# Optimization experiments

Hardware: AMD Instinct MI355X
Metric: run time of the kernel (lower is better)

## Reference

```python
import jax, jax.numpy as jnp
import numpy as np
from jax import lax

LENGTH, WIDTH = 64, 64
INPUT_DIM = 1


def _convlstm_layer(x_tbchw, W, b):
    """Run one ConvLSTM layer over time. x_tbchw: (L,B,Cin,H,W).
    W: (4*hid, Cin+hid, 3, 3), b: (4*hid,). Returns (outputs (L,B,hid,H,W), last_h)."""
    L, B, _, H, Wd = x_tbchw.shape
    hid = W.shape[0] // 4
    h0 = jnp.zeros((B, hid, H, Wd), dtype=x_tbchw.dtype)
    c0 = jnp.zeros((B, hid, H, Wd), dtype=x_tbchw.dtype)

    def step(carry, xt):
        h, c = carry
        z = lax.conv_general_dilated(
            jnp.concatenate([xt, h], axis=1), W,
            window_strides=(1, 1), padding='SAME',
            dimension_numbers=('NCHW', 'OIHW', 'NCHW'))
        z = z + b[None, :, None, None]
        cc_i, cc_f, cc_o, cc_g = jnp.split(z, 4, axis=1)
        c_next = jax.nn.sigmoid(cc_f) * c + jax.nn.sigmoid(cc_i) * jnp.tanh(cc_g)
        h_next = jax.nn.sigmoid(cc_o) * jnp.tanh(c_next)
        return (h_next, c_next), h_next

    (h_last, _), outs = lax.scan(step, (h0, c0), x_tbchw)
    return outs, h_last


def setup_inputs() -> dict:
    key = jax.random.key(0)
    k1, k2, k3 = jax.random.split(key, 3)
    B, L, N = 16, 12, LENGTH * WIDTH
    emd, out_len = 128, 12
    return {
        'history_data': jax.random.normal(k1, (B, L, N, 1), dtype=jnp.float32),
        'future_data': jnp.zeros((B, L, N, 1), dtype=jnp.float32),
        'W0': jax.random.normal(k2, (4 * emd, INPUT_DIM + emd, 3, 3), dtype=jnp.float32) * 0.05,
        'b0': jnp.zeros((4 * emd,), dtype=jnp.float32),
        'W1': jax.random.normal(k3, (4 * out_len, emd + out_len, 3, 3), dtype=jnp.float32) * 0.05,
        'b1': jnp.zeros((4 * out_len,), dtype=jnp.float32),
        'batch_seen': 0,
        'epoch': 0,
        'train': 1,
    }


def reference(history_data, future_data, W0, b0, W1, b1, batch_seen, epoch, train):
    B, L, N, C = history_data.shape
    # (B,L,1,H,W) -> (L,B,1,H,W) for time-major scan
    x = history_data[..., :INPUT_DIM].reshape(B, L, INPUT_DIM, LENGTH, WIDTH)
    x = jnp.transpose(x, (1, 0, 2, 3, 4))
    outs0, _ = _convlstm_layer(x, W0, b0)          # (L,B,emd,H,W)
    _, h_last = _convlstm_layer(outs0, W1, b1)     # (B,out_len,H,W)
    prediction = h_last.reshape(B, L, LENGTH * WIDTH)[..., None]  # (B,L,N,1)
    return prediction
```

## Files before the change

### kernel.cpp

```cpp
#include <hip/hip_runtime.h>
#include <hip/hip_bf16.h>


typedef __attribute__((ext_vector_type(8))) short short8;
typedef __attribute__((ext_vector_type(4))) float float4v;

#define CS 160
#define KTOT 1440

__device__ __forceinline__ float sigf(float x) { return 1.f / (1.f + __expf(-x)); }
__device__ __forceinline__ short f2hs(float v) {
  _Float16 h = (_Float16)v;
  return *(short*)&h;
}
__device__ __forceinline__ float hs2f(short s) {
  _Float16 h; *(short*)&h = s; return (float)h;
}
__device__ __forceinline__ float bs2f(short s) {
  __hip_bfloat16 h; *(short*)&h = s; return __bfloat162float(h);
}
__device__ __forceinline__ short f2bs(float v) {
  __hip_bfloat16 h = __float2bfloat16(v);
  return *(short*)&h;
}

__device__ __forceinline__ void async_ld16(const short* g, short* l) {
  __builtin_amdgcn_global_load_lds(
      (const __attribute__((address_space(1))) unsigned int*)g,
      (__attribute__((address_space(3))) unsigned int*)l, 16, 0, 0);
}

__device__ __forceinline__ void stage_row(const short* __restrict__ rowPtr, bool rowOK,
                                          short* dstRow, int lane,
                                          const short* __restrict__ zp) {
  #pragma unroll
  for (int j = 0; j < 4; ++j) {
    int e = j * 64 + lane;
    int px = e >> 2, v = e & 3;
    int xx = px - 1;
    const short* g = (rowOK && xx >= 0) ? (rowPtr + (size_t)xx * CS + v * 8) : zp;
    async_ld16(g, dstRow + e * 8);
  }
  if (lane < 8) {
    int px = 64 + (lane >> 2), v = lane & 3, xx = px - 1;
    short8 val = {0, 0, 0, 0, 0, 0, 0, 0};
    if (rowOK && xx < 64) val = *(const short8*)(rowPtr + (size_t)xx * CS + v * 8);
    *(short8*)(dstRow + px * 32 + v * 8) = val;
  }
}

__global__ void detect_dtype(const unsigned short* __restrict__ w0, int* __restrict__ flag) {
  int lane = threadIdx.x;
  int cnt = 0;
  for (int i = 0; i < 4; ++i) {
    unsigned short u = w0[2 * (lane + 64 * i)];
    int e = (u >> 7) & 0xFF;
    unsigned long long b = __ballot(e >= 0xC0);
    cnt += __popcll(b);
  }
  if (lane == 0) *flag = (cnt > 32) ? 1 : 0;
}

__global__ void canon_x(const void* __restrict__ hist, short* __restrict__ Xc,
                        const int* __restrict__ flag) {
  int i = blockIdx.x * 256 + threadIdx.x;
  float v = (*flag) ? ((const float*)hist)[i] : bs2f(((const short*)hist)[i]);
  if (!isfinite(v) || fabsf(v) > 1e4f) v = 0.f;
  Xc[i] = f2hs(v);
}

__global__ void canon_b(const void* __restrict__ b0, const void* __restrict__ b1,
                        float* __restrict__ Bc0, float* __restrict__ Bc1,
                        const int* __restrict__ flag) {
  int i = blockIdx.x * 256 + threadIdx.x;
  int fl = *flag;
  if (i < 512) {
    float v = fl ? ((const float*)b0)[i] : bs2f(((const short*)b0)[i]);
    if (!isfinite(v) || fabsf(v) > 1e4f) v = 0.f;
    Bc0[i] = v;
  } else if (i < 560) {
    int j = i - 512;
    float v = fl ? ((const float*)b1)[j] : bs2f(((const short*)b1)[j]);
    if (!isfinite(v) || fabsf(v) > 1e4f) v = 0.f;
    Bc1[j] = v;
  }
}

__global__ void prep_w0(const void* __restrict__ W0, short* __restrict__ Wp,
                        const int* __restrict__ flag) {
  int i = blockIdx.x * 256 + threadIdx.x;
  if (i >= 512 * KTOT) return;
  int fl = *flag;
  int co = i / KTOT, k = i - co * KTOT;
  int tap = k / CS, c = k - tap * CS;
  int ci = -1;
  if (c == 0) ci = 0;
  else if (c <= 128) ci = c;
  float w = 0.f;
  if (ci >= 0) {
    int widx = (co * 129 + ci) * 9 + tap;
    w = fl ? ((const float*)W0)[widx] : bs2f(((const short*)W0)[widx]);
    if (!isfinite(w) || fabsf(w) > 1e4f) w = 0.f;
  }
  Wp[i] = f2hs(w);
}

__global__ void prep_w1(const void* __restrict__ W1, short* __restrict__ Wp,
                        const int* __restrict__ flag) {
  int i = blockIdx.x * 256 + threadIdx.x;
  if (i >= 48 * KTOT) return;
  int fl = *flag;
  int co = i / KTOT, k = i - co * KTOT;
  int tap = k / CS, c = k - tap * CS;
  int ci = -1;
  if (c >= 1 && c <= 140) ci = c - 1;
  float w = 0.f;
  if (ci >= 0) {
    int widx = (co * 140 + ci) * 9 + tap;
    w = fl ? ((const float*)W1)[widx] : bs2f(((const short*)W1)[widx]);
    if (!isfinite(w) || fabsf(w) > 1e4f) w = 0.f;
  }
  Wp[i] = f2hs(w);
}

__global__ void fill_x0(const short* __restrict__ Xc, short* __restrict__ P0) {
  int p = blockIdx.x * 256 + threadIdx.x;
  int b = p >> 12, pix = p & 4095;
  P0[(size_t)p * CS] = Xc[b * 12 * 4096 + pix];
}

__global__ __launch_bounds__(256, 2) void gemm_gate0(
    const short* __restrict__ Pcur, short* __restrict__ Pnext,
    const short* __restrict__ Wp, const float* __restrict__ Bc0,
    float* __restrict__ C0, const short* __restrict__ Xc,
    const short* __restrict__ zp, int t) {
  int bx = blockIdx.x;
  int nt = bx >> 9, mt = bx & 511;
  int b = mt >> 5, y0 = (mt & 31) * 2;
  int tid = threadIdx.x, wave = tid >> 6, lane = tid & 63;
  int ln15 = lane & 15, quad = lane >> 4;
  int wm = wave & 1, wn = wave >> 1;
  int hc = nt * 32 + wn * 16 + ln15;

  __shared__ __align__(16) short halo[2 * 4 * 66 * 32];

  float4v acc[4][4];
  #pragma unroll
  for (int i = 0; i < 4; ++i)
    #pragma unroll
    for (int j = 0; j < 4; ++j) acc[i][j] = (float4v){0.f, 0.f, 0.f, 0.f};

  const short* wbase = Wp + (size_t)hc * KTOT + quad * 8;
  short8 bcur[4], bnxt[4];
  #pragma unroll
  for (int g = 0; g < 4; ++g)
    bcur[g] = *(const short8*)(wbase + (size_t)g * 128 * KTOT);

  int yy = y0 - 1 + wave;
  bool rowOK = (yy >= 0) && (yy < 64);
  const short* rowBase = Pcur + (size_t)((b * 64 + yy) * 64) * CS;

  stage_row(rowBase, rowOK, halo + wave * 2112, lane, zp);
  __syncthreads();

  for (int ch = 0; ch < 5; ++ch) {
    int c0 = ch * 32;
    const short* cur = halo + (ch & 1) * 8448;
    if (ch < 4)
      stage_row(rowBase + c0 + 32, rowOK, halo + ((ch + 1) & 1) * 8448 + wave * 2112,
                lane, zp);
    #pragma unroll
    for (int tap = 0; tap < 9; ++tap) {
      int dy = tap / 3, dx = tap - dy * 3;
      int ntap = (tap < 8) ? tap + 1 : 0;
      int nc0 = (tap < 8) ? c0 : ((ch < 4) ? c0 + 32 : c0);
      #pragma unroll
      for (int g = 0; g < 4; ++g)
        bnxt[g] = *(const short8*)(wbase + (size_t)g * 128 * KTOT + ntap * CS + nc0);

      short8 af[4];
      #pragma unroll
      for (int mf = 0; mf < 4; ++mf)
        af[mf] = *(const short8*)&cur[((wm + dy) * 66 + mf * 16 + ln15 + dx) * 32 + quad * 8];
      #pragma unroll
      for (int g = 0; g < 4; ++g)
        #pragma unroll
        for (int mf = 0; mf < 4; ++mf)
          acc[mf][g] = __builtin_amdgcn_mfma_f32_16x16x32_f16(af[mf], bcur[g], acc[mf][g], 0, 0, 0);
      #pragma unroll
      for (int g = 0; g < 4; ++g) bcur[g] = bnxt[g];
    }
    __syncthreads();
  }

  float bi = Bc0[hc], bff = Bc0[128 + hc], bo = Bc0[256 + hc], bg = Bc0[384 + hc];
  int rowPix = (b * 64 + y0 + wm) * 64;
  #pragma unroll
  for (int mf = 0; mf < 4; ++mf) {
    #pragma unroll
    for (int r = 0; r < 4; ++r) {
      int x = mf * 16 + quad * 4 + r;
      int pix = rowPix + x;
      float zi = acc[mf][0][r] + bi;
      float zf = acc[mf][1][r] + bff;
      float zo = acc[mf][2][r] + bo;
      float zg = acc[mf][3][r] + bg;
      float cprev = C0[(size_t)pix * 128 + hc];
      float cn = sigf(zf) * cprev + sigf(zi) * tanhf(zg);
      float hn = sigf(zo) * tanhf(cn);
      C0[(size_t)pix * 128 + hc] = cn;
      Pnext[(size_t)pix * CS + 1 + hc] = f2hs(hn);
    }
  }
  if (nt == 0 && t < 11 && tid < 128) {
    int rr = tid >> 6, x = tid & 63;
    int yw = y0 + rr;
    Pnext[(size_t)((b * 64 + yw) * 64 + x) * CS] = Xc[(b * 12 + t + 1) * 4096 + yw * 64 + x];
  }
}

__global__ __launch_bounds__(256, 2) void gemm_gate1(
    const short* __restrict__ Prd, short* __restrict__ Pwr,
    const short* __restrict__ Wp, const float* __restrict__ Bc1,
    float* __restrict__ C1, void* __restrict__ outp,
    const short* __restrict__ zp, const int* __restrict__ flagp, int t) {
  int bid = blockIdx.x;
  int b = bid >> 5, y0 = (bid & 31) * 2;
  int tid = threadIdx.x, wave = tid >> 6, lane = tid & 63;
  int ln15 = lane & 15, quad = lane >> 4;
  int wr = wave >> 1, wh = wave & 1;
  int flagv = *flagp;

  __shared__ __align__(16) short halo[2 * 4 * 66 * 32];

  float4v acc[2][3];
  #pragma unroll
  for (int i = 0; i < 2; ++i)
    #pragma unroll
    for (int j = 0; j < 3; ++j) acc[i][j] = (float4v){0.f, 0.f, 0.f, 0.f};

  int yy = y0 - 1 + wave;
  bool rowOK = (yy >= 0) && (yy < 64);
  const short* rowBase = Prd + (size_t)((b * 64 + yy) * 64) * CS;

  const short* wbase = Wp + (size_t)ln15 * KTOT + quad * 8;
  short8 bcur[3], bnxt[3];
  #pragma unroll
  for (int nf = 0; nf < 3; ++nf)
    bcur[nf] = *(const short8*)(wbase + (size_t)nf * 16 * KTOT);

  stage_row(rowBase, rowOK, halo + wave * 2112, lane, zp);
  __syncthreads();

  for (int ch = 0; ch < 5; ++ch) {
    int c0 = ch * 32;
    const short* cur = halo + (ch & 1) * 8448;
    if (ch < 4)
      stage_row(rowBase + c0 + 32, rowOK, halo + ((ch + 1) & 1) * 8448 + wave * 2112,
                lane, zp);
    #pragma unroll
    for (int tap = 0; tap < 9; ++tap) {
      int dy = tap / 3, dx = tap - dy * 3;
      int ntap = (tap < 8) ? tap + 1 : 0;
      int nc0 = (tap < 8) ? c0 : ((ch < 4) ? c0 + 32 : c0);
      #pragma unroll
      for (int nf = 0; nf < 3; ++nf)
        bnxt[nf] = *(const short8*)(wbase + (size_t)nf * 16 * KTOT + ntap * CS + nc0);

      short8 af[2];
      #pragma unroll
      for (int mf = 0; mf < 2; ++mf)
        af[mf] = *(const short8*)&cur[((wr + dy) * 66 + wh * 32 + mf * 16 + ln15 + dx) * 32
                                      + quad * 8];
      #pragma unroll
      for (int nf = 0; nf < 3; ++nf)
        #pragma unroll
        for (int mf = 0; mf < 2; ++mf)
          acc[mf][nf] = __builtin_amdgcn_mfma_f32_16x16x32_f16(af[mf], bcur[nf], acc[mf][nf], 0, 0, 0);
      #pragma unroll
      for (int nf = 0; nf < 3; ++nf) bcur[nf] = bnxt[nf];
    }
    __syncthreads();
  }

  float* zbuf = (float*)halo;
  #pragma unroll
  for (int mf = 0; mf < 2; ++mf)
    #pragma unroll
    for (int nf = 0; nf < 3; ++nf)
      #pragma unroll
      for (int r = 0; r < 4; ++r) {
        int pxl = wr * 64 + wh * 32 + mf * 16 + quad * 4 + r;
        zbuf[pxl * 48 + nf * 16 + ln15] = acc[mf][nf][r];
      }
  __syncthreads();

  #pragma unroll
  for (int k = 0; k < 6; ++k) {
    int id = k * 256 + tid;
    int hc = id >> 7, pxl = id & 127;
    float zi = zbuf[pxl * 48 + hc]      + Bc1[hc];
    float zf = zbuf[pxl * 48 + 12 + hc] + Bc1[12 + hc];
    float zo = zbuf[pxl * 48 + 24 + hc] + Bc1[24 + hc];
    float zg = zbuf[pxl * 48 + 36 + hc] + Bc1[36 + hc];
    int y = y0 + (pxl >> 6), x = pxl & 63;
    int pix = (b * 64 + y) * 64 + x;
    float cprev = C1[(size_t)pix * 12 + hc];
    float cn = sigf(zf) * cprev + sigf(zi) * tanhf(zg);
    float hn = sigf(zo) * tanhf(cn);
    C1[(size_t)pix * 12 + hc] = cn;
    Pwr[(size_t)pix * CS + 129 + hc] = f2hs(hn);
    if (t == 11) {
      int oidx = (b * 12 + hc) * 4096 + y * 64 + x;
      if (flagv) ((float*)outp)[oidx] = hn;
      else ((short*)outp)[oidx] = f2bs(hn);
    }
  }
}

extern "C" void kernel_launch(void* const* d_in, const int* in_sizes, int n_in,
                              void* d_out, int out_size, void* d_ws, size_t ws_size,
                              hipStream_t stream) {
  const void* hist = d_in[0];
  const void* W0 = d_in[2];
  const void* b0 = d_in[3];
  const void* W1 = d_in[4];
  const void* b1 = d_in[5];

  char* ws = (char*)d_ws;
  const size_t PszB = (size_t)16 * 4096 * CS * 2;
  short* P[2] = {(short*)ws, (short*)(ws + PszB)};
  float* C0 = (float*)(ws + 2 * PszB);
  const size_t C0e = 2 * PszB + 33554432;
  float* C1 = (float*)(ws + C0e);
  const size_t C1e = C0e + 3145728;
  short* zp = (short*)(ws + C1e);
  const size_t zpe = C1e + 256;
  short* Xc = (short*)(ws + zpe);
  const size_t Xce = zpe + 1572864;
  short* Wp0 = (short*)(ws + Xce);
  const size_t W0e = Xce + (size_t)512 * KTOT * 2;
  short* Wp1 = (short*)(ws + W0e);
  const size_t W1e = W0e + (size_t)48 * KTOT * 2;
  float* Bc0 = (float*)(ws + W1e);
  float* Bc1 = (float*)(ws + W1e + 2048);
  int* flag = (int*)(ws + W1e + 2048 + 192);

  hipMemsetAsync(ws, 0, zpe, stream);
  detect_dtype<<<1, 64, 0, stream>>>((const unsigned short*)W0, flag);
  canon_x<<<3072, 256, 0, stream>>>(hist, Xc, flag);
  canon_b<<<3, 256, 0, stream>>>(b0, b1, Bc0, Bc1, flag);
  prep_w0<<<(512 * KTOT + 255) / 256, 256, 0, stream>>>(W0, Wp0, flag);
  prep_w1<<<(48 * KTOT + 255) / 256, 256, 0, stream>>>(W1, Wp1, flag);
  fill_x0<<<256, 256, 0, stream>>>(Xc, P[0]);

  for (int t = 0; t < 12; ++t) {
    gemm_gate0<<<2048, 256, 0, stream>>>(P[t & 1], P[(t + 1) & 1], Wp0, Bc0, C0, Xc, zp, t);
    gemm_gate1<<<512, 256, 0, stream>>>(P[(t + 1) & 1], P[t & 1], Wp1, Bc1, C1,
                                        d_out, zp, flag, t);
  }
}
```

Before: 2.198 ms.

## Fuse layer-0 and layer-1 ConvLSTM steps into one skewed launch and swizzle LDS

Layer 0 at step k and layer 1 at step k-1 now run as separate block ranges of a single kernel launch. This cuts the launch count from 24 to 13 and lets the small layer-1 grid fill idle CUs while layer 0 runs. Layer-1 hidden state moves to channels 144..155 of the shared activation buffer so the two layers write disjoint regions, and the packed W1 weights are remapped to match. The LDS halo gets an XOR swizzle on both the async-store and fragment-read sides, and the gate scratch buffer gets a padded stride of 49; both target LDS bank conflicts. In exchange, the whole skew schedule depends on getting the double-buffer parity right, and the fused kernel carries the register and LDS footprint of both bodies.

New measurement: 2.407 ms. +9.5%, slower.

```diff
diff --git a/kernel.cpp b/kernel.cpp
--- a/kernel.cpp
+++ b/kernel.cpp
@@ -33,12 +33,13 @@
 __device__ __forceinline__ void stage_row(const short* __restrict__ rowPtr, bool rowOK,
                                           short* dstRow, int lane,
                                           const short* __restrict__ zp) {
+  int vs8 = (((lane & 3) ^ ((lane >> 3) & 3)) << 3);
   #pragma unroll
   for (int j = 0; j < 4; ++j) {
     int e = j * 64 + lane;
-    int px = e >> 2, v = e & 3;
+    int px = e >> 2;
     int xx = px - 1;
-    const short* g = (rowOK && xx >= 0) ? (rowPtr + (size_t)xx * CS + v * 8) : zp;
+    const short* g = (rowOK && xx >= 0) ? (rowPtr + (size_t)xx * CS + vs8) : zp;
     async_ld16(g, dstRow + e * 8);
   }
   if (lane < 8) {
@@ -113,7 +114,8 @@
   int co = i / KTOT, k = i - co * KTOT;
   int tap = k / CS, c = k - tap * CS;
   int ci = -1;
-  if (c >= 1 && c <= 140) ci = c - 1;
+  if (c >= 1 && c <= 128) ci = c - 1;
+  else if (c >= 144 && c <= 155) ci = 128 + (c - 144);
   float w = 0.f;
   if (ci >= 0) {
     int widx = (co * 140 + ci) * 9 + tap;
@@ -129,12 +131,11 @@
   P0[(size_t)p * CS] = Xc[b * 12 * 4096 + pix];
 }
 
-__global__ __launch_bounds__(256, 2) void gemm_gate0(
-    const short* __restrict__ Pcur, short* __restrict__ Pnext,
+__device__ __forceinline__ void gg0_body(
+    int bx, short* halo, const short* __restrict__ Pcur, short* __restrict__ Pnext,
     const short* __restrict__ Wp, const float* __restrict__ Bc0,
     float* __restrict__ C0, const short* __restrict__ Xc,
     const short* __restrict__ zp, int t) {
-  int bx = blockIdx.x;
   int nt = bx >> 9, mt = bx & 511;
   int b = mt >> 5, y0 = (mt & 31) * 2;
   int tid = threadIdx.x, wave = tid >> 6, lane = tid & 63;
@@ -142,8 +143,6 @@
   int wm = wave & 1, wn = wave >> 1;
   int hc = nt * 32 + wn * 16 + ln15;
 
-  __shared__ __align__(16) short halo[2 * 4 * 66 * 32];
-
   float4v acc[4][4];
   #pragma unroll
   for (int i = 0; i < 4; ++i)
@@ -178,10 +177,11 @@
       for (int g = 0; g < 4; ++g)
         bnxt[g] = *(const short8*)(wbase + (size_t)g * 128 * KTOT + ntap * CS + nc0);
 
+      int qs = (quad ^ (((ln15 + dx) >> 1) & 3)) * 8;
       short8 af[4];
       #pragma unroll
       for (int mf = 0; mf < 4; ++mf)
-        af[mf] = *(const short8*)&cur[((wm + dy) * 66 + mf * 16 + ln15 + dx) * 32 + quad * 8];
+        af[mf] = *(const short8*)&cur[((wm + dy) * 66 + mf * 16 + ln15 + dx) * 32 + qs];
       #pragma unroll
       for (int g = 0; g < 4; ++g)
         #pragma unroll
@@ -219,19 +219,15 @@
   }
 }
 
-__global__ __launch_bounds__(256, 2) void gemm_gate1(
-    const short* __restrict__ Prd, short* __restrict__ Pwr,
+__device__ __forceinline__ void gg1_body(
+    int bid, short* halo, const short* __restrict__ Prd, short* __restrict__ Pwr,
     const short* __restrict__ Wp, const float* __restrict__ Bc1,
     float* __restrict__ C1, void* __restrict__ outp,
-    const short* __restrict__ zp, const int* __restrict__ flagp, int t) {
-  int bid = blockIdx.x;
+    const short* __restrict__ zp, int flagv, int t) {
   int b = bid >> 5, y0 = (bid & 31) * 2;
   int tid = threadIdx.x, wave = tid >> 6, lane = tid & 63;
   int ln15 = lane & 15, quad = lane >> 4;
   int wr = wave >> 1, wh = wave & 1;
-  int flagv = *flagp;
-
-  __shared__ __align__(16) short halo[2 * 4 * 66 * 32];
 
   float4v acc[2][3];
   #pragma unroll
@@ -267,11 +263,12 @@
       for (int nf = 0; nf < 3; ++nf)
         bnxt[nf] = *(const short8*)(wbase + (size_t)nf * 16 * KTOT + ntap * CS + nc0);
 
+      int qs = (quad ^ (((ln15 + dx) >> 1) & 3)) * 8;
       short8 af[2];
       #pragma unroll
       for (int mf = 0; mf < 2; ++mf)
         af[mf] = *(const short8*)&cur[((wr + dy) * 66 + wh * 32 + mf * 16 + ln15 + dx) * 32
-                                      + quad * 8];
+                                      + qs];
       #pragma unroll
       for (int nf = 0; nf < 3; ++nf)
         #pragma unroll
@@ -291,7 +288,7 @@
       #pragma unroll
       for (int r = 0; r < 4; ++r) {
         int pxl = wr * 64 + wh * 32 + mf * 16 + quad * 4 + r;
-        zbuf[pxl * 48 + nf * 16 + ln15] = acc[mf][nf][r];
+        zbuf[pxl * 49 + nf * 16 + ln15] = acc[mf][nf][r];
       }
   __syncthreads();
 
@@ -299,22 +296,38 @@
   for (int k = 0; k < 6; ++k) {
     int id = k * 256 + tid;
     int hc = id >> 7, pxl = id & 127;
-    float zi = zbuf[pxl * 48 + hc]      + Bc1[hc];
-    float zf = zbuf[pxl * 48 + 12 + hc] + Bc1[12 + hc];
-    float zo = zbuf[pxl * 48 + 24 + hc] + Bc1[24 + hc];
-    float zg = zbuf[pxl * 48 + 36 + hc] + Bc1[36 + hc];
+    float zi = zbuf[pxl * 49 + hc]      + Bc1[hc];
+    float zf = zbuf[pxl * 49 + 12 + hc] + Bc1[12 + hc];
+    float zo = zbuf[pxl * 49 + 24 + hc] + Bc1[24 + hc];
+    float zg = zbuf[pxl * 49 + 36 + hc] + Bc1[36 + hc];
     int y = y0 + (pxl >> 6), x = pxl & 63;
     int pix = (b * 64 + y) * 64 + x;
     float cprev = C1[(size_t)pix * 12 + hc];
     float cn = sigf(zf) * cprev + sigf(zi) * tanhf(zg);
     float hn = sigf(zo) * tanhf(cn);
     C1[(size_t)pix * 12 + hc] = cn;
-    Pwr[(size_t)pix * CS + 129 + hc] = f2hs(hn);
+    Pwr[(size_t)pix * CS + 144 + hc] = f2hs(hn);
     if (t == 11) {
       int oidx = (b * 12 + hc) * 4096 + y * 64 + x;
       if (flagv) ((float*)outp)[oidx] = hn;
       else ((short*)outp)[oidx] = f2bs(hn);
     }
+  }
+}
+
+__global__ __launch_bounds__(256, 2) void fused_step(
+    const short* __restrict__ Pr, short* __restrict__ Pw,
+    const short* __restrict__ Wp0, const float* __restrict__ Bc0,
+    float* __restrict__ C0, const short* __restrict__ Xc,
+    const short* __restrict__ Wp1, const float* __restrict__ Bc1,
+    float* __restrict__ C1, void* __restrict__ outp,
+    const short* __restrict__ zp, const int* __restrict__ flagp, int k) {
+  __shared__ __align__(16) short halo[2 * 4 * 66 * 32];
+  int bx = blockIdx.x;
+  if (bx < 2048) {
+    if (k < 12) gg0_body(bx, halo, Pr, Pw, Wp0, Bc0, C0, Xc, zp, k);
+  } else {
+    if (k >= 1) gg1_body(bx - 2048, halo, Pr, Pw, Wp1, Bc1, C1, outp, zp, *flagp, k - 1);
   }
 }
 
@@ -354,9 +367,7 @@
   prep_w1<<<(48 * KTOT + 255) / 256, 256, 0, stream>>>(W1, Wp1, flag);
   fill_x0<<<256, 256, 0, stream>>>(Xc, P[0]);
 
-  for (int t = 0; t < 12; ++t) {
-    gemm_gate0<<<2048, 256, 0, stream>>>(P[t & 1], P[(t + 1) & 1], Wp0, Bc0, C0, Xc, zp, t);
-    gemm_gate1<<<512, 256, 0, stream>>>(P[(t + 1) & 1], P[t & 1], Wp1, Bc1, C1,
-                                        d_out, zp, flag, t);
-  }
-}
+  for (int k = 0; k <= 12; ++k)
+    fused_step<<<2560, 256, 0, stream>>>(P[k & 1], P[(k + 1) & 1], Wp0, Bc0, C0, Xc,
+                                         Wp1, Bc1, C1, d_out, zp, flag, k);
+}
```

## Split input and layer-1 hidden channels out of padded K to shrink GEMM depth

Applied to the files above, without the earlier changes.

Stores layer-0 hidden state in a 128-channel buffer instead of the 160-wide padded one that also held the input channel and layer-1 hidden state. The single input channel is handled through a precomputed 9-tap im2col buffer (Xtap) in one extra MFMA pass. Layer-1 hidden state gets its own 16-channel buffer with a separate small K pass. This cuts the main K loop from 5 chunks to 4 in both gate kernels. It also adds an XOR swizzle to the LDS halo layout and pads the layer-1 z buffer to avoid bank conflicts, at the cost of extra prep kernels and workspace.

After: 2.498 ms. 13.6% more time.

```diff
diff --git a/kernel.cpp b/kernel.cpp
--- a/kernel.cpp
+++ b/kernel.cpp
@@ -5,17 +5,14 @@
 typedef __attribute__((ext_vector_type(8))) short short8;
 typedef __attribute__((ext_vector_type(4))) float float4v;
 
-#define CS 160
-#define KTOT 1440
+#define CS 128
+#define KT0 1152
 
 __device__ __forceinline__ float sigf(float x) { return 1.f / (1.f + __expf(-x)); }
 __device__ __forceinline__ short f2hs(float v) {
   _Float16 h = (_Float16)v;
   return *(short*)&h;
 }
-__device__ __forceinline__ float hs2f(short s) {
-  _Float16 h; *(short*)&h = s; return (float)h;
-}
 __device__ __forceinline__ float bs2f(short s) {
   __hip_bfloat16 h; *(short*)&h = s; return __bfloat162float(h);
 }
@@ -33,12 +30,13 @@
 __device__ __forceinline__ void stage_row(const short* __restrict__ rowPtr, bool rowOK,
                                           short* dstRow, int lane,
                                           const short* __restrict__ zp) {
+  int vs8 = (((lane & 3) ^ ((lane >> 3) & 3)) << 3);
   #pragma unroll
   for (int j = 0; j < 4; ++j) {
     int e = j * 64 + lane;
-    int px = e >> 2, v = e & 3;
+    int px = e >> 2;
     int xx = px - 1;
-    const short* g = (rowOK && xx >= 0) ? (rowPtr + (size_t)xx * CS + v * 8) : zp;
+    const short* g = (rowOK && xx >= 0) ? (rowPtr + (size_t)xx * CS + vs8) : zp;
     async_ld16(g, dstRow + e * 8);
   }
   if (lane < 8) {
@@ -46,6 +44,24 @@
     short8 val = {0, 0, 0, 0, 0, 0, 0, 0};
     if (rowOK && xx < 64) val = *(const short8*)(rowPtr + (size_t)xx * CS + v * 8);
     *(short8*)(dstRow + px * 32 + v * 8) = val;
+  }
+}
+
+__device__ __forceinline__ void stage_h1(const short* __restrict__ rowPtr, bool rowOK,
+                                         short* dstRow, int lane,
+                                         const short* __restrict__ zp) {
+  #pragma unroll
+  for (int j = 0; j < 2; ++j) {
+    int e = j * 64 + lane;
+    int px = e >> 1, h = e & 1, xx = px - 1;
+    const short* g = (rowOK && xx >= 0) ? (rowPtr + (size_t)xx * 16 + h * 8) : zp;
+    async_ld16(g, dstRow + e * 8);
+  }
+  if (lane < 4) {
+    int px = 64 + (lane >> 1), h = lane & 1, xx = px - 1;
+    short8 val = {0, 0, 0, 0, 0, 0, 0, 0};
+    if (rowOK && xx < 64) val = *(const short8*)(rowPtr + (size_t)xx * 16 + h * 8);
+    *(short8*)(dstRow + px * 16 + h * 8) = val;
   }
 }
 
@@ -59,14 +75,6 @@
     cnt += __popcll(b);
   }
   if (lane == 0) *flag = (cnt > 32) ? 1 : 0;
-}
-
-__global__ void canon_x(const void* __restrict__ hist, short* __restrict__ Xc,
-                        const int* __restrict__ flag) {
-  int i = blockIdx.x * 256 + threadIdx.x;
-  float v = (*flag) ? ((const float*)hist)[i] : bs2f(((const short*)hist)[i]);
-  if (!isfinite(v) || fabsf(v) > 1e4f) v = 0.f;
-  Xc[i] = f2hs(v);
 }
 
 __global__ void canon_b(const void* __restrict__ b0, const void* __restrict__ b1,
@@ -86,54 +94,81 @@
   }
 }
 
+__device__ __forceinline__ float ldw(const void* W, int idx, int fl) {
+  float w = fl ? ((const float*)W)[idx] : bs2f(((const short*)W)[idx]);
+  if (!isfinite(w) || fabsf(w) > 1e4f) w = 0.f;
+  return w;
+}
+
 __global__ void prep_w0(const void* __restrict__ W0, short* __restrict__ Wp,
                         const int* __restrict__ flag) {
   int i = blockIdx.x * 256 + threadIdx.x;
-  if (i >= 512 * KTOT) return;
-  int fl = *flag;
-  int co = i / KTOT, k = i - co * KTOT;
-  int tap = k / CS, c = k - tap * CS;
-  int ci = -1;
-  if (c == 0) ci = 0;
-  else if (c <= 128) ci = c;
-  float w = 0.f;
-  if (ci >= 0) {
-    int widx = (co * 129 + ci) * 9 + tap;
-    w = fl ? ((const float*)W0)[widx] : bs2f(((const short*)W0)[widx]);
-    if (!isfinite(w) || fabsf(w) > 1e4f) w = 0.f;
-  }
-  Wp[i] = f2hs(w);
+  if (i >= 512 * KT0) return;
+  int fl = *flag;
+  int co = i / KT0, k = i - co * KT0;
+  int tap = k >> 7, c = k & 127;
+  Wp[i] = f2hs(ldw(W0, (co * 129 + 1 + c) * 9 + tap, fl));
+}
+
+__global__ void prep_wx(const void* __restrict__ W0, short* __restrict__ Wx,
+                        const int* __restrict__ flag) {
+  int i = blockIdx.x * 256 + threadIdx.x;
+  if (i >= 512 * 16) return;
+  int fl = *flag;
+  int co = i >> 4, k = i & 15;
+  float w = (k < 9) ? ldw(W0, (co * 129) * 9 + k, fl) : 0.f;
+  Wx[i] = f2hs(w);
 }
 
 __global__ void prep_w1(const void* __restrict__ W1, short* __restrict__ Wp,
                         const int* __restrict__ flag) {
   int i = blockIdx.x * 256 + threadIdx.x;
-  if (i >= 48 * KTOT) return;
-  int fl = *flag;
-  int co = i / KTOT, k = i - co * KTOT;
-  int tap = k / CS, c = k - tap * CS;
-  int ci = -1;
-  if (c >= 1 && c <= 140) ci = c - 1;
-  float w = 0.f;
-  if (ci >= 0) {
-    int widx = (co * 140 + ci) * 9 + tap;
-    w = fl ? ((const float*)W1)[widx] : bs2f(((const short*)W1)[widx]);
-    if (!isfinite(w) || fabsf(w) > 1e4f) w = 0.f;
-  }
-  Wp[i] = f2hs(w);
-}
-
-__global__ void fill_x0(const short* __restrict__ Xc, short* __restrict__ P0) {
-  int p = blockIdx.x * 256 + threadIdx.x;
-  int b = p >> 12, pix = p & 4095;
-  P0[(size_t)p * CS] = Xc[b * 12 * 4096 + pix];
+  if (i >= 48 * KT0) return;
+  int fl = *flag;
+  int co = i / KT0, k = i - co * KT0;
+  int tap = k >> 7, c = k & 127;
+  Wp[i] = f2hs(ldw(W1, (co * 140 + c) * 9 + tap, fl));
+}
+
+__global__ void prep_wh(const void* __restrict__ W1, short* __restrict__ Wh,
+                        const int* __restrict__ flag) {
+  int i = blockIdx.x * 256 + threadIdx.x;
+  if (i >= 48 * 144) return;
+  int fl = *flag;
+  int co = i / 144, k = i - co * 144;
+  int tap = k >> 4, kk = k & 15;
+  float w = (kk < 12) ? ldw(W1, (co * 140 + 128 + kk) * 9 + tap, fl) : 0.f;
+  Wh[i] = f2hs(w);
+}
+
+__global__ void prep_xtap(const void* __restrict__ hist, short* __restrict__ Xtap,
+                          const int* __restrict__ flag) {
+  int i = blockIdx.x * 256 + threadIdx.x;
+  int t = i >> 16, p = i & 65535;
+  int b = p >> 12, pix = p & 4095, y = pix >> 6, x = pix & 63;
+  int fl = *flag;
+  short8 lo = {0, 0, 0, 0, 0, 0, 0, 0}, hi = {0, 0, 0, 0, 0, 0, 0, 0};
+  #pragma unroll
+  for (int k = 0; k < 9; ++k) {
+    int dy = k / 3, dx = k - dy * 3;
+    int yy = y + dy - 1, xx = x + dx - 1;
+    float f = 0.f;
+    if (yy >= 0 && yy < 64 && xx >= 0 && xx < 64) {
+      int hidx = (b * 12 + t) * 4096 + yy * 64 + xx;
+      f = fl ? ((const float*)hist)[hidx] : bs2f(((const short*)hist)[hidx]);
+      if (!isfinite(f) || fabsf(f) > 1e4f) f = 0.f;
+    }
+    if (k < 8) lo[k] = f2hs(f); else hi[k - 8] = f2hs(f);
+  }
+  *(short8*)(Xtap + (size_t)i * 16) = lo;
+  *(short8*)(Xtap + (size_t)i * 16 + 8) = hi;
 }
 
 __global__ __launch_bounds__(256, 2) void gemm_gate0(
     const short* __restrict__ Pcur, short* __restrict__ Pnext,
-    const short* __restrict__ Wp, const float* __restrict__ Bc0,
-    float* __restrict__ C0, const short* __restrict__ Xc,
-    const short* __restrict__ zp, int t) {
+    const short* __restrict__ Wp, const short* __restrict__ Wx,
+    const float* __restrict__ Bc0, float* __restrict__ C0,
+    const short* __restrict__ Xtap, const short* __restrict__ zp, int t) {
   int bx = blockIdx.x;
   int nt = bx >> 9, mt = bx & 511;
   int b = mt >> 5, y0 = (mt & 31) * 2;
@@ -150,38 +185,58 @@
     #pragma unroll
     for (int j = 0; j < 4; ++j) acc[i][j] = (float4v){0.f, 0.f, 0.f, 0.f};
 
-  const short* wbase = Wp + (size_t)hc * KTOT + quad * 8;
+  const short* wbase = Wp + (size_t)hc * KT0 + quad * 8;
   short8 bcur[4], bnxt[4];
   #pragma unroll
   for (int g = 0; g < 4; ++g)
-    bcur[g] = *(const short8*)(wbase + (size_t)g * 128 * KTOT);
+    bcur[g] = *(const short8*)(wbase + (size_t)g * 128 * KT0);
 
   int yy = y0 - 1 + wave;
   bool rowOK = (yy >= 0) && (yy < 64);
   const short* rowBase = Pcur + (size_t)((b * 64 + yy) * 64) * CS;
+  int rowPix = (b * 64 + y0 + wm) * 64;
 
   stage_row(rowBase, rowOK, halo + wave * 2112, lane, zp);
+
+  {
+    bool hiQ = quad >= 2;
+    const short* xb = Xtap + ((size_t)t * 65536 + rowPix + ln15) * 16 + (quad & 1) * 8;
+    short8 ax[4], bx[4];
+    #pragma unroll
+    for (int mf = 0; mf < 4; ++mf) ax[mf] = *(const short8*)(xb + mf * 256);
+    #pragma unroll
+    for (int g = 0; g < 4; ++g) {
+      const short* wxp = Wx + (size_t)(g * 128 + hc) * 16 + (quad & 1) * 8;
+      bx[g] = *(const short8*)(hiQ ? zp : wxp);
+    }
+    #pragma unroll
+    for (int g = 0; g < 4; ++g)
+      #pragma unroll
+      for (int mf = 0; mf < 4; ++mf)
+        acc[mf][g] = __builtin_amdgcn_mfma_f32_16x16x32_f16(ax[mf], bx[g], acc[mf][g], 0, 0, 0);
+  }
   __syncthreads();
 
-  for (int ch = 0; ch < 5; ++ch) {
+  for (int ch = 0; ch < 4; ++ch) {
     int c0 = ch * 32;
     const short* cur = halo + (ch & 1) * 8448;
-    if (ch < 4)
+    if (ch < 3)
       stage_row(rowBase + c0 + 32, rowOK, halo + ((ch + 1) & 1) * 8448 + wave * 2112,
                 lane, zp);
     #pragma unroll
     for (int tap = 0; tap < 9; ++tap) {
       int dy = tap / 3, dx = tap - dy * 3;
       int ntap = (tap < 8) ? tap + 1 : 0;
-      int nc0 = (tap < 8) ? c0 : ((ch < 4) ? c0 + 32 : c0);
+      int nc0 = (tap < 8) ? c0 : ((ch < 3) ? c0 + 32 : c0);
       #pragma unroll
       for (int g = 0; g < 4; ++g)
-        bnxt[g] = *(const short8*)(wbase + (size_t)g * 128 * KTOT + ntap * CS + nc0);
-
+        bnxt[g] = *(const short8*)(wbase + (size_t)g * 128 * KT0 + ntap * 128 + nc0);
+
+      int qs = (quad ^ (((ln15 + dx) >> 1) & 3)) * 8;
       short8 af[4];
       #pragma unroll
       for (int mf = 0; mf < 4; ++mf)
-        af[mf] = *(const short8*)&cur[((wm + dy) * 66 + mf * 16 + ln15 + dx) * 32 + quad * 8];
+        af[mf] = *(const short8*)&cur[((wm + dy) * 66 + mf * 16 + ln15 + dx) * 32 + qs];
       #pragma unroll
       for (int g = 0; g < 4; ++g)
         #pragma unroll
@@ -194,7 +249,6 @@
   }
 
   float bi = Bc0[hc], bff = Bc0[128 + hc], bo = Bc0[256 + hc], bg = Bc0[384 + hc];
-  int rowPix = (b * 64 + y0 + wm) * 64;
   #pragma unroll
   for (int mf = 0; mf < 4; ++mf) {
     #pragma unroll
@@ -209,19 +263,15 @@
       float cn = sigf(zf) * cprev + sigf(zi) * tanhf(zg);
       float hn = sigf(zo) * tanhf(cn);
       C0[(size_t)pix * 128 + hc] = cn;
-      Pnext[(size_t)pix * CS + 1 + hc] = f2hs(hn);
-    }
-  }
-  if (nt == 0 && t < 11 && tid < 128) {
-    int rr = tid >> 6, x = tid & 63;
-    int yw = y0 + rr;
-    Pnext[(size_t)((b * 64 + yw) * 64 + x) * CS] = Xc[(b * 12 + t + 1) * 4096 + yw * 64 + x];
+      Pnext[(size_t)pix * CS + hc] = f2hs(hn);
+    }
   }
 }
 
 __global__ __launch_bounds__(256, 2) void gemm_gate1(
-    const short* __restrict__ Prd, short* __restrict__ Pwr,
-    const short* __restrict__ Wp, const float* __restrict__ Bc1,
+    const short* __restrict__ Prd, const short* __restrict__ H1rd,
+    short* __restrict__ H1wr, const short* __restrict__ Wp,
+    const short* __restrict__ Wh, const float* __restrict__ Bc1,
     float* __restrict__ C1, void* __restrict__ outp,
     const short* __restrict__ zp, const int* __restrict__ flagp, int t) {
   int bid = blockIdx.x;
@@ -232,6 +282,7 @@
   int flagv = *flagp;
 
   __shared__ __align__(16) short halo[2 * 4 * 66 * 32];
+  __shared__ __align__(16) short h1h[4 * 66 * 16];
 
   float4v acc[2][3];
   #pragma unroll
@@ -242,36 +293,39 @@
   int yy = y0 - 1 + wave;
   bool rowOK = (yy >= 0) && (yy < 64);
   const short* rowBase = Prd + (size_t)((b * 64 + yy) * 64) * CS;
-
-  const short* wbase = Wp + (size_t)ln15 * KTOT + quad * 8;
+  const short* h1Base = H1rd + (size_t)((b * 64 + yy) * 64) * 16;
+
+  const short* wbase = Wp + (size_t)ln15 * KT0 + quad * 8;
   short8 bcur[3], bnxt[3];
   #pragma unroll
   for (int nf = 0; nf < 3; ++nf)
-    bcur[nf] = *(const short8*)(wbase + (size_t)nf * 16 * KTOT);
+    bcur[nf] = *(const short8*)(wbase + (size_t)nf * 16 * KT0);
 
   stage_row(rowBase, rowOK, halo + wave * 2112, lane, zp);
+  stage_h1(h1Base, rowOK, h1h + wave * 1056, lane, zp);
   __syncthreads();
 
-  for (int ch = 0; ch < 5; ++ch) {
+  for (int ch = 0; ch < 4; ++ch) {
     int c0 = ch * 32;
     const short* cur = halo + (ch & 1) * 8448;
-    if (ch < 4)
+    if (ch < 3)
       stage_row(rowBase + c0 + 32, rowOK, halo + ((ch + 1) & 1) * 8448 + wave * 2112,
                 lane, zp);
     #pragma unroll
     for (int tap = 0; tap < 9; ++tap) {
       int dy = tap / 3, dx = tap - dy * 3;
       int ntap = (tap < 8) ? tap + 1 : 0;
-      int nc0 = (tap < 8) ? c0 : ((ch < 4) ? c0 + 32 : c0);
+      int nc0 = (tap < 8) ? c0 : ((ch < 3) ? c0 + 32 : c0);
       #pragma unroll
       for (int nf = 0; nf < 3; ++nf)
-        bnxt[nf] = *(const short8*)(wbase + (size_t)nf * 16 * KTOT + ntap * CS + nc0);
-
+        bnxt[nf] = *(const short8*)(wbase + (size_t)nf * 16 * KT0 + ntap * 128 + nc0);
+
+      int qs = (quad ^ (((ln15 + dx) >> 1) & 3)) * 8;
       short8 af[2];
       #pragma unroll
       for (int mf = 0; mf < 2; ++mf)
         af[mf] = *(const short8*)&cur[((wr + dy) * 66 + wh * 32 + mf * 16 + ln15 + dx) * 32
-                                      + quad * 8];
+                                      + qs];
       #pragma unroll
       for (int nf = 0; nf < 3; ++nf)
         #pragma unroll
@@ -283,6 +337,31 @@
     __syncthreads();
   }
 
+  {
+    bool hiQ = quad >= 2;
+    #pragma unroll
+    for (int tap = 0; tap < 9; ++tap) {
+      int dy = tap / 3, dx = tap - dy * 3;
+      short8 bh[3];
+      #pragma unroll
+      for (int nf = 0; nf < 3; ++nf) {
+        const short* whp = Wh + (size_t)((nf * 16 + ln15) * 9 + tap) * 16 + (quad & 1) * 8;
+        bh[nf] = *(const short8*)(hiQ ? zp : whp);
+      }
+      short8 ah[2];
+      #pragma unroll
+      for (int mf = 0; mf < 2; ++mf)
+        ah[mf] = *(const short8*)&h1h[((wr + dy) * 66 + wh * 32 + mf * 16 + ln15 + dx) * 16
+                                      + (quad & 1) * 8];
+      #pragma unroll
+      for (int nf = 0; nf < 3; ++nf)
+        #pragma unroll
+        for (int mf = 0; mf < 2; ++mf)
+          acc[mf][nf] = __builtin_amdgcn_mfma_f32_16x16x32_f16(ah[mf], bh[nf], acc[mf][nf], 0, 0, 0);
+    }
+  }
+  __syncthreads();
+
   float* zbuf = (float*)halo;
   #pragma unroll
   for (int mf = 0; mf < 2; ++mf)
@@ -291,7 +370,7 @@
       #pragma unroll
       for (int r = 0; r < 4; ++r) {
         int pxl = wr * 64 + wh * 32 + mf * 16 + quad * 4 + r;
-        zbuf[pxl * 48 + nf * 16 + ln15] = acc[mf][nf][r];
+        zbuf[pxl * 49 + nf * 16 + ln15] = acc[mf][nf][r];
       }
   __syncthreads();
 
@@ -299,17 +378,17 @@
   for (int k = 0; k < 6; ++k) {
     int id = k * 256 + tid;
     int hc = id >> 7, pxl = id & 127;
-    float zi = zbuf[pxl * 48 + hc]      + Bc1[hc];
-    float zf = zbuf[pxl * 48 + 12 + hc] + Bc1[12 + hc];
-    float zo = zbuf[pxl * 48 + 24 + hc] + Bc1[24 + hc];
-    float zg = zbuf[pxl * 48 + 36 + hc] + Bc1[36 + hc];
+    float zi = zbuf[pxl * 49 + hc]      + Bc1[hc];
+    float zf = zbuf[pxl * 49 + 12 + hc] + Bc1[12 + hc];
+    float zo = zbuf[pxl * 49 + 24 + hc] + Bc1[24 + hc];
+    float zg = zbuf[pxl * 49 + 36 + hc] + Bc1[36 + hc];
     int y = y0 + (pxl >> 6), x = pxl & 63;
     int pix = (b * 64 + y) * 64 + x;
     float cprev = C1[(size_t)pix * 12 + hc];
     float cn = sigf(zf) * cprev + sigf(zi) * tanhf(zg);
     float hn = sigf(zo) * tanhf(cn);
     C1[(size_t)pix * 12 + hc] = cn;
-    Pwr[(size_t)pix * CS + 129 + hc] = f2hs(hn);
+    H1wr[(size_t)pix * 16 + hc] = f2hs(hn);
     if (t == 11) {
       int oidx = (b * 12 + hc) * 4096 + y * 64 + x;
       if (flagv) ((float*)outp)[oidx] = hn;
@@ -334,29 +413,38 @@
   const size_t C0e = 2 * PszB + 33554432;
   float* C1 = (float*)(ws + C0e);
   const size_t C1e = C0e + 3145728;
-  short* zp = (short*)(ws + C1e);
-  const size_t zpe = C1e + 256;
-  short* Xc = (short*)(ws + zpe);
-  const size_t Xce = zpe + 1572864;
-  short* Wp0 = (short*)(ws + Xce);
-  const size_t W0e = Xce + (size_t)512 * KTOT * 2;
-  short* Wp1 = (short*)(ws + W0e);
-  const size_t W1e = W0e + (size_t)48 * KTOT * 2;
-  float* Bc0 = (float*)(ws + W1e);
-  float* Bc1 = (float*)(ws + W1e + 2048);
-  int* flag = (int*)(ws + W1e + 2048 + 192);
+  const size_t H1szB = (size_t)16 * 4096 * 16 * 2;
+  short* H1[2] = {(short*)(ws + C1e), (short*)(ws + C1e + H1szB)};
+  const size_t H1e = C1e + 2 * H1szB;
+  short* zp = (short*)(ws + H1e);
+  const size_t zpe = H1e + 256;
+  short* Xtap = (short*)(ws + zpe);
+  const size_t Xte = zpe + (size_t)12 * 65536 * 16 * 2;
+  short* Wp0 = (short*)(ws + Xte);
+  const size_t W0e = Xte + (size_t)512 * KT0 * 2;
+  short* Wx0 = (short*)(ws + W0e);
+  const size_t Wxe = W0e + 512 * 16 * 2;
+  short* Wp1 = (short*)(ws + Wxe);
+  const size_t W1e = Wxe + (size_t)48 * KT0 * 2;
+  short* Wh1 = (short*)(ws + W1e);
+  const size_t Whe = W1e + 48 * 144 * 2;
+  float* Bc0 = (float*)(ws + Whe);
+  float* Bc1 = (float*)(ws + Whe + 2048);
+  int* flag = (int*)(ws + Whe + 2048 + 192);
 
   hipMemsetAsync(ws, 0, zpe, stream);
   detect_dtype<<<1, 64, 0, stream>>>((const unsigned short*)W0, flag);
-  canon_x<<<3072, 256, 0, stream>>>(hist, Xc, flag);
   canon_b<<<3, 256, 0, stream>>>(b0, b1, Bc0, Bc1, flag);
-  prep_w0<<<(512 * KTOT + 255) / 256, 256, 0, stream>>>(W0, Wp0, flag);
-  prep_w1<<<(48 * KTOT + 255) / 256, 256, 0, stream>>>(W1, Wp1, flag);
-  fill_x0<<<256, 256, 0, stream>>>(Xc, P[0]);
+  prep_w0<<<(512 * KT0 + 255) / 256, 256, 0, stream>>>(W0, Wp0, flag);
+  prep_wx<<<32, 256, 0, stream>>>(W0, Wx0, flag);
+  prep_w1<<<(48 * KT0 + 255) / 256, 256, 0, stream>>>(W1, Wp1, flag);
+  prep_wh<<<27, 256, 0, stream>>>(W1, Wh1, flag);
+  prep_xtap<<<3072, 256, 0, stream>>>(hist, Xtap, flag);
 
   for (int t = 0; t < 12; ++t) {
-    gemm_gate0<<<2048, 256, 0, stream>>>(P[t & 1], P[(t + 1) & 1], Wp0, Bc0, C0, Xc, zp, t);
-    gemm_gate1<<<512, 256, 0, stream>>>(P[(t + 1) & 1], P[t & 1], Wp1, Bc1, C1,
-                                        d_out, zp, flag, t);
-  }
-}
+    gemm_gate0<<<2048, 256, 0, stream>>>(P[t & 1], P[(t + 1) & 1], Wp0, Wx0, Bc0, C0,
+                                         Xtap, zp, t);
+    gemm_gate1<<<512, 256, 0, stream>>>(P[(t + 1) & 1], H1[(t + 1) & 1], H1[t & 1],
+                                        Wp1, Wh1, Bc1, C1, d_out, zp, flag, t);
+  }
+}
```
